# Kernel tuning notes

Measured on AMD Instinct MI355X. Metric: run time of the kernel, lower is better.

The kernel has to match this reference:

```python
import jax, jax.numpy as jnp
import numpy as np
import math

IMAGE_SIZE = 300
STEPS = [16, 32, 64, 100, 150, 300]
MIN_SIZES = [60, 105, 150, 195, 240, 285]
MAX_SIZES = [105, 150, 195, 240, 285, 330]
ASPECT_RATIOS = [2, 3]
SCORE_THRESH = 0.02
NMS_THRESH = 0.45
POST_NMS_TOP_N = 100
VAR_XY, VAR_WH = 0.1, 0.2
BATCH, NUM_CLASSES = 16, 201


def _make_priors():
    # SSD-style anchor generation in (cx, cy, w, h), relative coords.
    priors = []
    for k, step in enumerate(STEPS):
        f = math.ceil(IMAGE_SIZE / step)
        s = MIN_SIZES[k] / IMAGE_SIZE
        sp = math.sqrt(MIN_SIZES[k] * MAX_SIZES[k]) / IMAGE_SIZE
        for i in range(f):
            for j in range(f):
                cx = (j + 0.5) * step / IMAGE_SIZE
                cy = (i + 0.5) * step / IMAGE_SIZE
                priors.append([cx, cy, s, s])
                priors.append([cx, cy, sp, sp])
                for ar in ASPECT_RATIOS:
                    r = math.sqrt(ar)
                    priors.append([cx, cy, s * r, s / r])
                    priors.append([cx, cy, s / r, s * r])
    return np.asarray(priors, dtype=np.float32)  # [3000, 4]


def setup_inputs() -> dict:
    key = jax.random.key(0)
    k1, k2 = jax.random.split(key)
    priors = jnp.asarray(_make_priors())  # [P, 4]
    P = priors.shape[0]
    pred_bbox_deltas = jax.random.normal(k1, (BATCH, P, 4), dtype=jnp.float32)
    objectness = jax.random.normal(k2, (BATCH, P, NUM_CLASSES), dtype=jnp.float32)
    return {"pred_bbox_deltas": pred_bbox_deltas, "objectness": objectness, "priors": priors}


def reference(pred_bbox_deltas, objectness, priors):
    # Eval path of MultiBoxHeads.filter_priors: softmax -> box decode ->
    # score filter -> class-aware (batched) NMS -> top-N, padded to fixed size.
    P = priors.shape[0]
    C = objectness.shape[-1]
    probs = jax.nn.softmax(objectness, axis=-1)  # [B, P, C]

    # BoxCoder.decode with variances (0.1, 0.2); priors are (cx, cy, w, h).
    pxy, pwh = priors[:, :2], priors[:, 2:]
    xy = pred_bbox_deltas[..., :2] * VAR_XY * pwh + pxy  # [B, P, 2]
    wh = jnp.exp(pred_bbox_deltas[..., 2:] * VAR_WH) * pwh
    decoded = jnp.concatenate([xy - 0.5 * wh, xy + 0.5 * wh], axis=-1)  # [B, P, 4] xyxy

    # Per-candidate class labels (background class 0 dropped), shared across images.
    labels = jnp.broadcast_to(jnp.arange(1, C), (P, C - 1)).reshape(-1)  # [P*(C-1)] int

    def nms_image(dec, prob):
        scores = prob[:, 1:].reshape(-1)  # [P*(C-1)]
        boxes = jnp.broadcast_to(dec[:, None, :], (P, C - 1, 4)).reshape(-1, 4)
        s = jnp.where(scores > SCORE_THRESH, scores, -1.0)
        # batched_nms trick: offset boxes by label so classes never overlap.
        off = jnp.max(boxes) + 1.0
        bo = boxes + labels.astype(boxes.dtype)[:, None] * off
        areas = (bo[:, 2] - bo[:, 0]) * (bo[:, 3] - bo[:, 1])

        def step(s, _):
            i = jnp.argmax(s)
            sc = s[i]
            b = bo[i]
            ix1 = jnp.maximum(bo[:, 0], b[0])
            iy1 = jnp.maximum(bo[:, 1], b[1])
            ix2 = jnp.minimum(bo[:, 2], b[2])
            iy2 = jnp.minimum(bo[:, 3], b[3])
            inter = jnp.clip(ix2 - ix1, 0.0) * jnp.clip(iy2 - iy1, 0.0)
            iou = inter / (areas + areas[i] - inter)
            s = jnp.where(iou > NMS_THRESH, -1.0, s).at[i].set(-1.0)
            return s, (i, sc)

        _, (idx, sc) = jax.lax.scan(step, s, None, length=POST_NMS_TOP_N)
        ok = sc > SCORE_THRESH  # slots that hold real detections
        b_out = jnp.where(ok[:, None], jnp.clip(boxes[idx], 0.0, 1.0), 0.0)  # parse() clamp
        s_out = jnp.where(ok, sc, 0.0)
        l_out = jnp.where(ok, labels[idx].astype(boxes.dtype), 0.0)
        # [K, 6] = (x1, y1, x2, y2, score, label); zero rows are padding.
        return jnp.concatenate([b_out, s_out[:, None], l_out[:, None]], axis=-1)

    return jax.vmap(nms_image)(decoded, probs)  # [B, POST_NMS_TOP_N, 6]
```

## Files before the change

kernel.cpp:

```cpp
#include <hip/hip_runtime.h>
#include <cfloat>
#include <cstdint>

#define BATCH 16
#define PRIORS 3000
#define NCLS 201
#define NLBL 200
#define TOPN 100
#define SCORE_THR 0.02f
#define NMS_THR 0.45f

#define FPPB 16
#define FBLK ((PRIORS + FPPB - 1) / FPPB)
#define SEGW 64
#define SEGS (FBLK * 4)
#define SLOTS (SEGS * SEGW)
#define HOTW 8
#define OVF_CAP 1024
#define T0 0.08f

#define NMS_T 1024
#define NBINS 1024
#define HCAP 512
#define SB_BASE 0x3CA3

__device__ __forceinline__ int key_stratum(uint64_t k) {
    int s = (int)(k >> 48) - SB_BASE;
    return s < 0 ? 0 : (s > NBINS - 1 ? NBINS - 1 : s);
}

__device__ __forceinline__ void softmax4(
    const float* __restrict__ obj, int b, int pbase, int lane,
    bool pv[4], float e0[4], float e1[4], float e2[4], float e3[4],
    float inv[4])
{
    float v0[4], v1[4], v2[4], v3[4];
#pragma unroll
    for (int pp = 0; pp < 4; ++pp) {
        int p = pbase + pp;
        pv[pp] = (p < PRIORS);
        const float* x = obj + ((size_t)b * PRIORS + (pv[pp] ? p : PRIORS - 1)) * NCLS;
        v0[pp] = x[lane];
        v1[pp] = x[lane + 64];
        v2[pp] = x[lane + 128];
        v3[pp] = (lane + 192 < NCLS) ? x[lane + 192] : -FLT_MAX;
    }
    float mx[4];
#pragma unroll
    for (int pp = 0; pp < 4; ++pp)
        mx[pp] = fmaxf(fmaxf(v0[pp], v1[pp]), fmaxf(v2[pp], v3[pp]));
    for (int d = 32; d > 0; d >>= 1) {
#pragma unroll
        for (int pp = 0; pp < 4; ++pp)
            mx[pp] = fmaxf(mx[pp], __shfl_xor(mx[pp], d, 64));
    }
    float se[4];
#pragma unroll
    for (int pp = 0; pp < 4; ++pp) {
        e0[pp] = expf(v0[pp] - mx[pp]);
        e1[pp] = expf(v1[pp] - mx[pp]);
        e2[pp] = expf(v2[pp] - mx[pp]);
        e3[pp] = (lane + 192 < NCLS) ? expf(v3[pp] - mx[pp]) : 0.0f;
        se[pp] = e0[pp] + e1[pp] + e2[pp] + e3[pp];
    }
    for (int d = 32; d > 0; d >>= 1) {
#pragma unroll
        for (int pp = 0; pp < 4; ++pp)
            se[pp] += __shfl_xor(se[pp], d, 64);
    }
#pragma unroll
    for (int pp = 0; pp < 4; ++pp) inv[pp] = 1.0f / se[pp];
}

__global__ __launch_bounds__(256) void score_filter_kernel(
    const float* __restrict__ obj,
    uint64_t*    __restrict__ hotS,
    int*         __restrict__ flags)
{
    const int b    = blockIdx.y;
    const int wave = threadIdx.x >> 6;
    const int lane = threadIdx.x & 63;
    const int segId = blockIdx.x * 4 + wave;
    uint64_t* myhot = hotS + ((size_t)b * SEGS + segId) * HOTW;
    const int pbase = blockIdx.x * FPPB + wave * 4;

    bool pv[4]; float e0[4], e1[4], e2[4], e3[4], inv[4];
    softmax4(obj, b, pbase, lane, pv, e0, e1, e2, e3, inv);

    int hcur = 0;
#pragma unroll
    for (int pp = 0; pp < 4; ++pp) {
        float ev[4] = { e0[pp], e1[pp], e2[pp], e3[pp] };
#pragma unroll
        for (int k = 0; k < 4; ++k) {
            int c = lane + 64 * k;
            float prob = ev[k] * inv[pp];
            bool hotp = pv[pp] && (c >= 1) && (c < NCLS) && (prob > T0);
            uint64_t hmask = __ballot(hotp);
            if (hotp) {
                uint32_t oid = (uint32_t)((pbase + pp) * NLBL + (c - 1));
                uint64_t key = ((uint64_t)__float_as_uint(prob) << 32)
                             | (uint64_t)(0xFFFFFFFFu - oid);
                int hidx = hcur + (int)__popcll(hmask & ((1ull << lane) - 1ull));
                if (hidx < HOTW) myhot[hidx] = key;
                else flags[b] = 1;
            }
            hcur += (int)__popcll(hmask);
        }
    }
    if (lane < HOTW && lane >= (hcur < HOTW ? hcur : HOTW)) myhot[lane] = 0ull;
}

__device__ __forceinline__ void sort512_desc(const uint64_t* skey,
                                             uint64_t K[8], int lane)
{
#pragma unroll
    for (int r = 0; r < 8; ++r) K[r] = skey[r * 64 + lane];
#pragma unroll
    for (int k2 = 2; k2 <= 512; k2 <<= 1) {
#pragma unroll
        for (int j2 = k2 >> 1; j2 >= 64; j2 >>= 1) {
            int j2r = j2 >> 6;
#pragma unroll
            for (int r = 0; r < 8; ++r) {
                if ((r & j2r) == 0) {
                    int rp = r | j2r;
                    bool up = ((((r << 6) + lane) & k2) == 0);
                    uint64_t a = K[r], bb = K[rp];
                    uint64_t mxk = a > bb ? a : bb;
                    uint64_t mnk = a > bb ? bb : a;
                    K[r]  = up ? mxk : mnk;
                    K[rp] = up ? mnk : mxk;
                }
            }
        }
#pragma unroll
        for (int j2 = ((k2 >> 1) < 32 ? (k2 >> 1) : 32); j2 >= 1; j2 >>= 1) {
#pragma unroll
            for (int r = 0; r < 8; ++r) {
                uint64_t o = __shfl_xor((unsigned long long)K[r], j2, 64);
                bool up = ((((r << 6) + lane) & k2) == 0);
                bool lower = ((lane & j2) == 0);
                K[r] = (up == lower) ? (K[r] > o ? K[r] : o)
                                     : (K[r] < o ? K[r] : o);
            }
        }
    }
}

__device__ __forceinline__ int scan_sorted_w0(
    const uint64_t K[8], int b, const float4* __restrict__ dbox, float ofb,
    float4* abox, float* aarea, int na, float* __restrict__ out, int lane)
{
#pragma unroll
    for (int r = 0; r < 8; ++r) {
        if (na >= TOPN) break;
        uint64_t myk = K[r];
        bool valid = (myk != 0ull);
        uint32_t oid = 0xFFFFFFFFu - (uint32_t)myk;
        int p = valid ? (int)(oid / NLBL) : 0;
        int c = valid ? ((int)(oid - (uint32_t)p * NLBL) + 1) : 1;
        float4 db = dbox[p];
        float lof = (float)c * ofb;
        float qx1 = db.x + lof, qy1 = db.y + lof;
        float qx2 = db.z + lof, qy2 = db.w + lof;
        float aq = (qx2 - qx1) * (qy2 - qy1);
        bool dead = false;
        for (int l = 0; l < na; ++l) {
            float4 a = abox[l];
            float ix1 = fmaxf(qx1, a.x), iy1 = fmaxf(qy1, a.y);
            float ix2 = fminf(qx2, a.z), iy2 = fminf(qy2, a.w);
            float inter = fmaxf(ix2 - ix1, 0.0f) * fmaxf(iy2 - iy1, 0.0f);
            float iou = inter / (aq + aarea[l] - inter);
            if (iou > NMS_THR) dead = true;
        }
        uint64_t alive = __ballot(valid && !dead);
        while (alive != 0ull && na < TOPN) {
            int j = __ffsll((unsigned long long)alive) - 1;
            float ax1 = __shfl(qx1, j, 64);
            float ay1 = __shfl(qy1, j, 64);
            float ax2 = __shfl(qx2, j, 64);
            float ay2 = __shfl(qy2, j, 64);
            float aa  = __shfl(aq,  j, 64);
            if (lane == j) {
                abox[na]  = make_float4(qx1, qy1, qx2, qy2);
                aarea[na] = aq;
                float* o = out + ((size_t)b * TOPN + na) * 6;
                o[0] = fminf(fmaxf(db.x, 0.0f), 1.0f);
                o[1] = fminf(fmaxf(db.y, 0.0f), 1.0f);
                o[2] = fminf(fmaxf(db.z, 0.0f), 1.0f);
                o[3] = fminf(fmaxf(db.w, 0.0f), 1.0f);
                o[4] = __uint_as_float((uint32_t)(myk >> 32));
                o[5] = (float)c;
            }
            na++;
            bool mine = ((alive >> lane) & 1ull) != 0ull;
            bool drop = (lane == j);
            if (mine && !drop) {
                float ix1 = fmaxf(qx1, ax1), iy1 = fmaxf(qy1, ay1);
                float ix2 = fminf(qx2, ax2), iy2 = fminf(qy2, ay2);
                float inter = fmaxf(ix2 - ix1, 0.0f) * fmaxf(iy2 - iy1, 0.0f);
                float iou = inter / (aq + aa - inter);
                if (iou > NMS_THR) drop = true;
            }
            alive = __ballot(mine && !drop);
        }
    }
    return na;
}

__device__ __forceinline__ int scan_step_w0(
    uint64_t key, int b, const float4* __restrict__ dbox, float ofb,
    float4* abox, float* aarea, int na, float* __restrict__ out, int lane)
{
    uint32_t oid = 0xFFFFFFFFu - (uint32_t)key;
    int p = (int)(oid / NLBL);
    int c = (int)(oid - (uint32_t)p * NLBL) + 1;
    float4 db = dbox[p];
    float lo = (float)c * ofb;
    float qx1 = db.x + lo, qy1 = db.y + lo;
    float qx2 = db.z + lo, qy2 = db.w + lo;
    float aq = (qx2 - qx1) * (qy2 - qy1);
    bool sup = false;
    for (int l = lane; l < na; l += 64) {
        float4 a = abox[l];
        float ix1 = fmaxf(qx1, a.x), iy1 = fmaxf(qy1, a.y);
        float ix2 = fminf(qx2, a.z), iy2 = fminf(qy2, a.w);
        float inter = fmaxf(ix2 - ix1, 0.0f) * fmaxf(iy2 - iy1, 0.0f);
        float iou = inter / (aq + aarea[l] - inter);
        if (iou > NMS_THR) sup = true;
    }
    if (__ballot(sup) == 0ull) {
        if (lane == 0) {
            abox[na]  = make_float4(qx1, qy1, qx2, qy2);
            aarea[na] = aq;
            float* o = out + ((size_t)b * TOPN + na) * 6;
            o[0] = fminf(fmaxf(db.x, 0.0f), 1.0f);
            o[1] = fminf(fmaxf(db.y, 0.0f), 1.0f);
            o[2] = fminf(fmaxf(db.z, 0.0f), 1.0f);
            o[3] = fminf(fmaxf(db.w, 0.0f), 1.0f);
            o[4] = __uint_as_float((uint32_t)(key >> 32));
            o[5] = (float)c;
        }
        __threadfence_block();
        return na + 1;
    }
    return na;
}

__global__ __launch_bounds__(NMS_T) void nms_kernel(
    const float*    __restrict__ deltas,
    const float*    __restrict__ priors,
    const float*    __restrict__ obj,
    const uint64_t* __restrict__ hotS,
    const int*      __restrict__ flags,
    uint64_t*       __restrict__ segWS,
    uint64_t*       __restrict__ ovfWS,
    float*          __restrict__ out)
{
    __shared__ float4   dbox[PRIORS];
    __shared__ int      sufx[NBINS];
    __shared__ uint64_t skey[HCAP];
    __shared__ float4   qbox[HCAP];
    __shared__ float    qarea[HCAP];
    __shared__ uint64_t adjB[8 * HCAP];
    __shared__ float4   abox[112];
    __shared__ float    aarea[112];
    __shared__ uint64_t rk[NMS_T / 64];
    __shared__ float    wredF[NMS_T / 64];
    __shared__ int      wtotS[NMS_T / 64];
    __shared__ int      carryS[NMS_T / 64];
    __shared__ int cntC, ovfC, loS, naS;
    __shared__ uint64_t fkS;

    const int b    = blockIdx.x;
    const int tid  = threadIdx.x;
    const int wave = tid >> 6;
    const int lane = tid & 63;
    const uint64_t* hslots = hotS + (size_t)b * SEGS * HOTW;
    uint64_t* slots = segWS + (size_t)b * SLOTS;
    uint64_t* ovfp  = ovfWS + (size_t)b * OVF_CAP;

    if (tid == 0) { cntC = 0; naS = 0; }
    if (lane == 0) wredF[wave] = -FLT_MAX;
    __syncthreads();

    for (int j = tid; j < SEGS * HOTW; j += NMS_T) {
        uint64_t k = (j < SEGS * HOTW) ? hslots[j] : 0ull;
        uint64_t m = __ballot(k != 0ull);
        if (m) {
            int base = 0;
            if (lane == 0) base = atomicAdd(&cntC, (int)__popcll(m));
            base = __shfl(base, 0, 64);
            if (k) {
                int i = base + (int)__popcll(m & ((1ull << lane) - 1ull));
                if (i < HCAP) skey[i] = k;
            }
        }
    }
    __syncthreads();
    int hc = cntC;
    bool fast = (flags[b] == 0) && (hc <= HCAP);
    bool decoded = false;

    if (fast) {
        if (tid < HCAP && tid >= hc) skey[tid] = 0ull;
        __syncthreads();
        if (wave == 0) {
            uint64_t K[8];
            sort512_desc(skey, K, lane);
#pragma unroll
            for (int r = 0; r < 8; ++r) skey[r * 64 + lane] = K[r];
        } else {
            int base0 = (wave - 1) * 200;
            float lmax = -FLT_MAX;
            for (int p = base0 + lane; p < base0 + 200; p += 64) {
                float4 d4 = ((const float4*)deltas)[(size_t)b * PRIORS + p];
                float4 pr = ((const float4*)priors)[p];
                float cx = d4.x * 0.1f * pr.z + pr.x;
                float cy = d4.y * 0.1f * pr.w + pr.y;
                float w  = expf(d4.z * 0.2f) * pr.z;
                float h  = expf(d4.w * 0.2f) * pr.w;
                float x1 = cx - 0.5f * w, y1 = cy - 0.5f * h;
                float x2 = cx + 0.5f * w, y2 = cy + 0.5f * h;
                dbox[p] = make_float4(x1, y1, x2, y2);
                lmax = fmaxf(lmax, fmaxf(fmaxf(x1, y1), fmaxf(x2, y2)));
            }
            for (int d = 32; d > 0; d >>= 1)
                lmax = fmaxf(lmax, __shfl_xor(lmax, d, 64));
            if (lane == 0) wredF[wave] = lmax;
        }
        decoded = true;
        __syncthreads();

        float v = wredF[lane & 15];
        for (int d = 8; d > 0; d >>= 1) v = fmaxf(v, __shfl_xor(v, d, 64));
        float ofb = v + 1.0f;

        if (tid < HCAP) {
            uint64_t k = skey[tid];
            bool valid = (k != 0ull);
            uint32_t oid = 0xFFFFFFFFu - (uint32_t)k;
            int p = valid ? (int)(oid / NLBL) : 0;
            int c = valid ? ((int)(oid - (uint32_t)p * NLBL) + 1) : 1;
            float4 db = dbox[p];
            float lof = (float)c * ofb;
            float4 q = make_float4(db.x + lof, db.y + lof,
                                   db.z + lof, db.w + lof);
            qbox[tid]  = q;
            qarea[tid] = (q.z - q.x) * (q.w - q.y);
        }
        for (int i = tid; i < 8 * HCAP; i += NMS_T) adjB[i] = 0ull;
        __syncthreads();

        int hcw = (hc + 63) >> 6;
        int P2  = (hcw * (hcw + 1)) >> 1;
        for (int pair = wave; pair < P2; pair += NMS_T / 64) {
            int wj = 0;
            while ((((wj + 1) * (wj + 2)) >> 1) <= pair) ++wj;
            int wi = pair - ((wj * (wj + 1)) >> 1);
            int j  = (wj << 6) + lane;
            float4 qj = qbox[j];
            float  aj = qarea[j];
            int ib = wi << 6;
            uint64_t m = 0ull;
#pragma unroll 8
            for (int i = 0; i < 64; ++i) {
                float4 qi = qbox[ib + i];
                float ix1 = fmaxf(qj.x, qi.x), iy1 = fmaxf(qj.y, qi.y);
                float ix2 = fminf(qj.z, qi.z), iy2 = fminf(qj.w, qi.w);
                float inter = fmaxf(ix2 - ix1, 0.0f) * fmaxf(iy2 - iy1, 0.0f);
                float iou = inter / (aj + qarea[ib + i] - inter);
                m |= (uint64_t)(iou > NMS_THR) << i;
            }
            if (wi == wj)
                m &= (lane == 63) ? ~0ull : ((1ull << (lane + 1)) - 1ull);
            adjB[wi * HCAP + j] = m;
        }
        if (wave == 0 && lane < 8) rk[lane] = 0ull;
        __syncthreads();

        if (wave == 0) {
            uint64_t accwA[8];
#pragma unroll
            for (int w = 0; w < 8; ++w) accwA[w] = 0ull;
            int na = 0;
#pragma unroll
            for (int w = 0; w < 8; ++w) {
                if (w < hcw && na < TOPN) {
                    int nInW = hc - (w << 6);
                    uint64_t init = (nInW >= 64) ? ~0ull
                                  : (nInW > 0 ? ((1ull << nInW) - 1ull) : 0ull);
                    uint64_t deadOr = 0ull;
#pragma unroll
                    for (int wp = 0; wp < w; ++wp)
                        deadOr |= adjB[wp * HCAP + (w << 6) + lane] & accwA[wp];
                    uint64_t mycol = adjB[w * HCAP + (w << 6) + lane];
                    uint64_t rem = init & ~__ballot(deadOr != 0ull);
                    uint64_t acc = 0ull;
                    while (rem != 0ull && na < TOPN) {
                        int rr = __ffsll((unsigned long long)rem) - 1;
                        acc |= 1ull << rr;
                        ++na;
                        rem &= ~__ballot(((mycol >> rr) & 1ull) != 0ull);
                    }
                    accwA[w] = acc;
                    if (lane == 0) rk[w] = acc;
                }
            }
            if (lane == 0) naS = na;
        }
        __syncthreads();

        if (tid < HCAP) {
            int w = tid >> 6, rr = tid & 63;
            uint64_t aw = rk[w];
            if ((aw >> rr) & 1ull) {
                int idx = (int)__popcll(aw & ((1ull << rr) - 1ull));
                for (int k = 0; k < w; ++k) idx += (int)__popcll(rk[k]);
                uint64_t myk = skey[tid];
                uint32_t oid = 0xFFFFFFFFu - (uint32_t)myk;
                int p = (int)(oid / NLBL);
                int c = (int)(oid - (uint32_t)p * NLBL) + 1;
                float4 db = dbox[p];
                float* o = out + ((size_t)b * TOPN + idx) * 6;
                o[0] = fminf(fmaxf(db.x, 0.0f), 1.0f);
                o[1] = fminf(fmaxf(db.y, 0.0f), 1.0f);
                o[2] = fminf(fmaxf(db.z, 0.0f), 1.0f);
                o[3] = fminf(fmaxf(db.w, 0.0f), 1.0f);
                o[4] = __uint_as_float((uint32_t)(myk >> 32));
                o[5] = (float)c;
            }
        }
        __syncthreads();
    }

    if (naS < TOPN) {
        if (tid == 0) ovfC = 0;
        __syncthreads();
        for (int u = wave; u < SEGS; u += NMS_T / 64) {
            int fb = u >> 2, vw = u & 3;
            int pbase = fb * FPPB + vw * 4;
            uint64_t* myseg = slots + (size_t)u * SEGW;
            bool pv[4]; float e0[4], e1[4], e2[4], e3[4], inv[4];
            softmax4(obj, b, pbase, lane, pv, e0, e1, e2, e3, inv);
            int cursor = 0;
#pragma unroll
            for (int pp = 0; pp < 4; ++pp) {
                float ev[4] = { e0[pp], e1[pp], e2[pp], e3[pp] };
#pragma unroll
                for (int k = 0; k < 4; ++k) {
                    int c = lane + 64 * k;
                    float prob = ev[k] * inv[pp];
                    bool pass = pv[pp] && (c >= 1) && (c < NCLS) && (prob > SCORE_THR);
                    uint64_t mask = __ballot(pass);
                    if (pass) {
                        uint32_t oid = (uint32_t)((pbase + pp) * NLBL + (c - 1));
                        uint64_t key = ((uint64_t)__float_as_uint(prob) << 32)
                                     | (uint64_t)(0xFFFFFFFFu - oid);
                        int idx = cursor + (int)__popcll(mask & ((1ull << lane) - 1ull));
                        if (idx < SEGW) {
                            myseg[idx] = key;
                        } else {
                            int gi = atomicAdd(&ovfC, 1);
                            if (gi < OVF_CAP) ovfp[gi] = key;
                        }
                    }
                    cursor += (int)__popcll(mask);
                }
            }
            if (lane >= (cursor < SEGW ? cursor : SEGW)) myseg[lane] = 0ull;
        }
        __threadfence_block();
        __syncthreads();
        int n_ovf = ovfC; if (n_ovf > OVF_CAP) n_ovf = OVF_CAP;

        if (!decoded) {
            float lmax = -FLT_MAX;
            for (int p = tid; p < PRIORS; p += NMS_T) {
                float4 d4 = ((const float4*)deltas)[(size_t)b * PRIORS + p];
                float4 pr = ((const float4*)priors)[p];
                float cx = d4.x * 0.1f * pr.z + pr.x;
                float cy = d4.y * 0.1f * pr.w + pr.y;
                float w  = expf(d4.z * 0.2f) * pr.z;
                float h  = expf(d4.w * 0.2f) * pr.w;
                float x1 = cx - 0.5f * w, y1 = cy - 0.5f * h;
                float x2 = cx + 0.5f * w, y2 = cy + 0.5f * h;
                dbox[p] = make_float4(x1, y1, x2, y2);
                lmax = fmaxf(lmax, fmaxf(fmaxf(x1, y1), fmaxf(x2, y2)));
            }
            for (int d = 32; d > 0; d >>= 1)
                lmax = fmaxf(lmax, __shfl_xor(lmax, d, 64));
            if (lane == 0) wredF[wave] = lmax;
        }
        sufx[tid] = 0;
        if (tid == 0) naS = 0;
        __syncthreads();
        for (int j = tid; j < SLOTS; j += NMS_T) {
            uint64_t k = slots[j];
            if (k) atomicAdd(&sufx[key_stratum(k)], 1);
        }
        for (int j = tid; j < n_ovf; j += NMS_T) {
            uint64_t k = ovfp[j];
            if (k) atomicAdd(&sufx[key_stratum(k)], 1);
        }
        __syncthreads();
        {
            int v = sufx[64 * wave + lane];
            int s = v;
            for (int d = 1; d < 64; d <<= 1) {
                int t = __shfl_down(s, d, 64);
                if (lane + d < 64) s += t;
            }
            if (lane == 0) wtotS[wave] = s;
            __syncthreads();
            if (wave == 0 && lane < NMS_T / 64) {
                int tv = wtotS[lane];
                int ts = tv;
                for (int d = 1; d < NMS_T / 64; d <<= 1) {
                    int t = __shfl_down(ts, d, 64);
                    if (lane + d < NMS_T / 64) ts += t;
                }
                carryS[lane] = ts - tv;
            }
            __syncthreads();
            sufx[64 * wave + lane] = s + carryS[wave];
        }
        int curHi = NBINS;
        for (;;) {
            __syncthreads();
            int naCur = naS;
            int A = (curHi < NBINS) ? sufx[curHi] : 0;
            int remaining = sufx[0] - A;
            if (naCur >= TOPN || remaining <= 0 || curHi <= 0) break;
            int target = A + HCAP;
            if (tid == 0) { loS = curHi; cntC = 0; }
            __syncthreads();
            if (tid < curHi) {
                if (sufx[tid] <= target && (tid == 0 || sufx[tid - 1] > target))
                    loS = tid;
            }
            __syncthreads();
            int lo = loS;

            if (lo < curHi) {
                for (int j = tid; j < SLOTS; j += NMS_T) {
                    uint64_t k = slots[j];
                    if (k) {
                        int s = key_stratum(k);
                        if (s >= lo && s < curHi) {
                            int i = atomicAdd(&cntC, 1);
                            if (i < HCAP) skey[i] = k;
                        }
                    }
                }
                for (int j = tid; j < n_ovf; j += NMS_T) {
                    uint64_t k = ovfp[j];
                    if (k) {
                        int s = key_stratum(k);
                        if (s >= lo && s < curHi) {
                            int i = atomicAdd(&cntC, 1);
                            if (i < HCAP) skey[i] = k;
                        }
                    }
                }
                __syncthreads();
                if (tid < HCAP && tid >= cntC) skey[tid] = 0ull;
                __syncthreads();
                if (wave == 0) {
                    uint64_t K[8];
                    sort512_desc(skey, K, lane);
                    float ofb;
                    {
                        float v = (lane < NMS_T / 64) ? wredF[lane] : -FLT_MAX;
                        for (int d = 32; d > 0; d >>= 1) v = fmaxf(v, __shfl_xor(v, d, 64));
                        ofb = v + 1.0f;
                    }
                    int na = scan_sorted_w0(K, b, dbox, ofb, abox, aarea, naS, out, lane);
                    if (lane == 0) naS = na;
                }
                curHi = lo;
            } else {
                float ofbT;
                {
                    float v = (lane < NMS_T / 64) ? wredF[lane] : -FLT_MAX;
                    for (int d = 32; d > 0; d >>= 1) v = fmaxf(v, __shfl_xor(v, d, 64));
                    ofbT = v + 1.0f;
                }
                int s = curHi - 1;
                uint64_t lastK = ~0ull;
                for (;;) {
                    __syncthreads();
                    if (naS >= TOPN) break;
                    uint64_t bk = 0ull;
                    for (int j = tid; j < SLOTS; j += NMS_T) {
                        uint64_t k = slots[j];
                        if (k && key_stratum(k) == s && k < lastK && k > bk) bk = k;
                    }
                    for (int j = tid; j < n_ovf; j += NMS_T) {
                        uint64_t k = ovfp[j];
                        if (k && key_stratum(k) == s && k < lastK && k > bk) bk = k;
                    }
                    for (int d = 32; d > 0; d >>= 1) {
                        uint64_t o = __shfl_xor((unsigned long long)bk, d, 64);
                        bk = (o > bk) ? o : bk;
                    }
                    if (lane == 0) rk[wave] = bk;
                    __syncthreads();
                    if (tid == 0) {
                        uint64_t fk = rk[0];
                        for (int w = 1; w < NMS_T / 64; ++w) fk = (rk[w] > fk) ? rk[w] : fk;
                        fkS = fk;
                    }
                    __syncthreads();
                    uint64_t fk = fkS;
                    if (fk == 0ull) break;
                    if (wave == 0) {
                        int nal = naS;
                        nal = scan_step_w0(fk, b, dbox, ofbT, abox, aarea, nal, out, lane);
                        if (lane == 0) naS = nal;
                    }
                    lastK = fk;
                }
                curHi = s;
            }
        }
    }
    __syncthreads();
    int naF = naS;
    for (int idx = tid; idx < (TOPN - naF) * 6; idx += NMS_T)
        out[(size_t)b * TOPN * 6 + (size_t)naF * 6 + idx] = 0.0f;
}

extern "C" void kernel_launch(void* const* d_in, const int* in_sizes, int n_in,
                              void* d_out, int out_size, void* d_ws, size_t ws_size,
                              hipStream_t stream)
{
    const float* deltas = (const float*)d_in[0];
    const float* obj    = (const float*)d_in[1];
    const float* priors = (const float*)d_in[2];
    float* out = (float*)d_out;

    char* ws = (char*)d_ws;
    int*      flags = (int*)ws;
    uint64_t* hotA  = (uint64_t*)(ws + 256);
    uint64_t* segA  = hotA + (size_t)BATCH * SEGS * HOTW;
    uint64_t* ovfA  = segA + (size_t)BATCH * SLOTS;

    hipMemsetAsync(ws, 0, 64, stream);
    dim3 fg(FBLK, BATCH, 1);
    score_filter_kernel<<<fg, 256, 0, stream>>>(obj, hotA, flags);
    nms_kernel<<<BATCH, NMS_T, 0, stream>>>(deltas, priors, obj, hotA, flags,
                                            segA, ovfA, out);
}
```

Before: 125.5 us.

## Fuse score filter and NMS into one kernel with last-block election

Merges the softmax/score-filter kernel and the per-image NMS kernel into a single launch. Each block filters 64 priors with 1024 threads, then an atomic counter per image elects the last finishing block to run NMS, removing a kernel launch boundary. To fit shared memory, the decoded box array is dropped on the fast path (boxes are recomputed from global deltas/priors when needed) and a union buffer is shared between the slow-path decoded boxes and the adjacency/query arrays. The NMS tail now runs in whichever block finishes last, and the fast path pays extra global loads and exp per box lookup.

```diff
diff --git a/kernel.cpp b/kernel.cpp
--- a/kernel.cpp
+++ b/kernel.cpp
@@ -10,10 +10,11 @@
 #define SCORE_THR 0.02f
 #define NMS_THR 0.45f
 
-#define FPPB 16
-#define FBLK ((PRIORS + FPPB - 1) / FPPB)
+#define PPB 64
+#define FBLK2 ((PRIORS + PPB - 1) / PPB)
+#define WPB 16
 #define SEGW 64
-#define SEGS (FBLK * 4)
+#define SEGS (FBLK2 * WPB)
 #define SLOTS (SEGS * SEGW)
 #define HOTW 8
 #define OVF_CAP 1024
@@ -27,6 +28,20 @@
 __device__ __forceinline__ int key_stratum(uint64_t k) {
     int s = (int)(k >> 48) - SB_BASE;
     return s < 0 ? 0 : (s > NBINS - 1 ? NBINS - 1 : s);
+}
+
+__device__ __forceinline__ float4 decode_box(
+    const float* __restrict__ deltas, const float* __restrict__ priors,
+    int b, int p)
+{
+    float4 d4 = ((const float4*)deltas)[(size_t)b * PRIORS + p];
+    float4 pr = ((const float4*)priors)[p];
+    float cx = d4.x * 0.1f * pr.z + pr.x;
+    float cy = d4.y * 0.1f * pr.w + pr.y;
+    float w  = expf(d4.z * 0.2f) * pr.z;
+    float h  = expf(d4.w * 0.2f) * pr.w;
+    return make_float4(cx - 0.5f * w, cy - 0.5f * h,
+                       cx + 0.5f * w, cy + 0.5f * h);
 }
 
 __device__ __forceinline__ void softmax4(
@@ -70,45 +85,6 @@
     }
 #pragma unroll
     for (int pp = 0; pp < 4; ++pp) inv[pp] = 1.0f / se[pp];
-}
-
-__global__ __launch_bounds__(256) void score_filter_kernel(
-    const float* __restrict__ obj,
-    uint64_t*    __restrict__ hotS,
-    int*         __restrict__ flags)
-{
-    const int b    = blockIdx.y;
-    const int wave = threadIdx.x >> 6;
-    const int lane = threadIdx.x & 63;
-    const int segId = blockIdx.x * 4 + wave;
-    uint64_t* myhot = hotS + ((size_t)b * SEGS + segId) * HOTW;
-    const int pbase = blockIdx.x * FPPB + wave * 4;
-
-    bool pv[4]; float e0[4], e1[4], e2[4], e3[4], inv[4];
-    softmax4(obj, b, pbase, lane, pv, e0, e1, e2, e3, inv);
-
-    int hcur = 0;
-#pragma unroll
-    for (int pp = 0; pp < 4; ++pp) {
-        float ev[4] = { e0[pp], e1[pp], e2[pp], e3[pp] };
-#pragma unroll
-        for (int k = 0; k < 4; ++k) {
-            int c = lane + 64 * k;
-            float prob = ev[k] * inv[pp];
-            bool hotp = pv[pp] && (c >= 1) && (c < NCLS) && (prob > T0);
-            uint64_t hmask = __ballot(hotp);
-            if (hotp) {
-                uint32_t oid = (uint32_t)((pbase + pp) * NLBL + (c - 1));
-                uint64_t key = ((uint64_t)__float_as_uint(prob) << 32)
-                             | (uint64_t)(0xFFFFFFFFu - oid);
-                int hidx = hcur + (int)__popcll(hmask & ((1ull << lane) - 1ull));
-                if (hidx < HOTW) myhot[hidx] = key;
-                else flags[b] = 1;
-            }
-            hcur += (int)__popcll(hmask);
-        }
-    }
-    if (lane < HOTW && lane >= (hcur < HOTW ? hcur : HOTW)) myhot[lane] = 0ull;
 }
 
 __device__ __forceinline__ void sort512_desc(const uint64_t* skey,
@@ -149,7 +125,7 @@
 }
 
 __device__ __forceinline__ int scan_sorted_w0(
-    const uint64_t K[8], int b, const float4* __restrict__ dbox, float ofb,
+    const uint64_t K[8], int b, const float4* dbox, float ofb,
     float4* abox, float* aarea, int na, float* __restrict__ out, int lane)
 {
 #pragma unroll
@@ -210,7 +186,7 @@
 }
 
 __device__ __forceinline__ int scan_step_w0(
-    uint64_t key, int b, const float4* __restrict__ dbox, float ofb,
+    uint64_t key, int b, const float4* dbox, float ofb,
     float4* abox, float* aarea, int na, float* __restrict__ out, int lane)
 {
     uint32_t oid = 0xFFFFFFFFu - (uint32_t)key;
@@ -248,35 +224,78 @@
     return na;
 }
 
-__global__ __launch_bounds__(NMS_T) void nms_kernel(
+__global__ __launch_bounds__(NMS_T) void fused_kernel(
     const float*    __restrict__ deltas,
     const float*    __restrict__ priors,
     const float*    __restrict__ obj,
-    const uint64_t* __restrict__ hotS,
-    const int*      __restrict__ flags,
+    uint64_t*       __restrict__ hotS,
+    int*            __restrict__ flags,
+    int*            __restrict__ done,
     uint64_t*       __restrict__ segWS,
     uint64_t*       __restrict__ ovfWS,
     float*          __restrict__ out)
 {
-    __shared__ float4   dbox[PRIORS];
+    __shared__ __align__(16) char uMem[48 * 1024];
+    uint64_t* adjB  = (uint64_t*)uMem;
+    float4*   qbox  = (float4*)(uMem + 32 * 1024);
+    float*    qarea = (float*)(uMem + 40 * 1024);
+    float4*   dboxF = (float4*)uMem;
+    __shared__ uint64_t skey[HCAP];
     __shared__ int      sufx[NBINS];
-    __shared__ uint64_t skey[HCAP];
-    __shared__ float4   qbox[HCAP];
-    __shared__ float    qarea[HCAP];
-    __shared__ uint64_t adjB[8 * HCAP];
     __shared__ float4   abox[112];
     __shared__ float    aarea[112];
     __shared__ uint64_t rk[NMS_T / 64];
     __shared__ float    wredF[NMS_T / 64];
     __shared__ int      wtotS[NMS_T / 64];
     __shared__ int      carryS[NMS_T / 64];
-    __shared__ int cntC, ovfC, loS, naS;
+    __shared__ int cntC, ovfC, loS, naS, electedS;
     __shared__ uint64_t fkS;
 
-    const int b    = blockIdx.x;
+    const int b    = blockIdx.y;
     const int tid  = threadIdx.x;
     const int wave = tid >> 6;
     const int lane = tid & 63;
+
+    {
+        const int segId = blockIdx.x * WPB + wave;
+        const int pbase = blockIdx.x * PPB + wave * 4;
+        uint64_t* myhot = hotS + ((size_t)b * SEGS + segId) * HOTW;
+
+        bool pv[4]; float e0[4], e1[4], e2[4], e3[4], inv[4];
+        softmax4(obj, b, pbase, lane, pv, e0, e1, e2, e3, inv);
+
+        int hcur = 0;
+#pragma unroll
+        for (int pp = 0; pp < 4; ++pp) {
+            float ev[4] = { e0[pp], e1[pp], e2[pp], e3[pp] };
+#pragma unroll
+            for (int k = 0; k < 4; ++k) {
+                int c = lane + 64 * k;
+                float prob = ev[k] * inv[pp];
+                bool hotp = pv[pp] && (c >= 1) && (c < NCLS) && (prob > T0);
+                uint64_t hmask = __ballot(hotp);
+                if (hotp) {
+                    uint32_t oid = (uint32_t)((pbase + pp) * NLBL + (c - 1));
+                    uint64_t key = ((uint64_t)__float_as_uint(prob) << 32)
+                                 | (uint64_t)(0xFFFFFFFFu - oid);
+                    int hidx = hcur + (int)__popcll(hmask & ((1ull << lane) - 1ull));
+                    if (hidx < HOTW) myhot[hidx] = key;
+                    else flags[b] = 1;
+                }
+                hcur += (int)__popcll(hmask);
+            }
+        }
+        if (lane < HOTW && lane >= (hcur < HOTW ? hcur : HOTW)) myhot[lane] = 0ull;
+    }
+
+    __threadfence();
+    __syncthreads();
+    if (tid == 0)
+        electedS = (atomicAdd(&done[b], 1) == FBLK2 - 1) ? 1 : 0;
+    __syncthreads();
+    if (!electedS) return;
+    __threadfence();
+
     const uint64_t* hslots = hotS + (size_t)b * SEGS * HOTW;
     uint64_t* slots = segWS + (size_t)b * SLOTS;
     uint64_t* ovfp  = ovfWS + (size_t)b * OVF_CAP;
@@ -286,7 +305,7 @@
     __syncthreads();
 
     for (int j = tid; j < SEGS * HOTW; j += NMS_T) {
-        uint64_t k = (j < SEGS * HOTW) ? hslots[j] : 0ull;
+        uint64_t k = hslots[j];
         uint64_t m = __ballot(k != 0ull);
         if (m) {
             int base = 0;
@@ -301,7 +320,6 @@
     __syncthreads();
     int hc = cntC;
     bool fast = (flags[b] == 0) && (hc <= HCAP);
-    bool decoded = false;
 
     if (fast) {
         if (tid < HCAP && tid >= hc) skey[tid] = 0ull;
@@ -315,22 +333,13 @@
             int base0 = (wave - 1) * 200;
             float lmax = -FLT_MAX;
             for (int p = base0 + lane; p < base0 + 200; p += 64) {
-                float4 d4 = ((const float4*)deltas)[(size_t)b * PRIORS + p];
-                float4 pr = ((const float4*)priors)[p];
-                float cx = d4.x * 0.1f * pr.z + pr.x;
-                float cy = d4.y * 0.1f * pr.w + pr.y;
-                float w  = expf(d4.z * 0.2f) * pr.z;
-                float h  = expf(d4.w * 0.2f) * pr.w;
-                float x1 = cx - 0.5f * w, y1 = cy - 0.5f * h;
-                float x2 = cx + 0.5f * w, y2 = cy + 0.5f * h;
-                dbox[p] = make_float4(x1, y1, x2, y2);
-                lmax = fmaxf(lmax, fmaxf(fmaxf(x1, y1), fmaxf(x2, y2)));
+                float4 d = decode_box(deltas, priors, b, p);
+                lmax = fmaxf(lmax, fmaxf(fmaxf(d.x, d.y), fmaxf(d.z, d.w)));
             }
             for (int d = 32; d > 0; d >>= 1)
                 lmax = fmaxf(lmax, __shfl_xor(lmax, d, 64));
             if (lane == 0) wredF[wave] = lmax;
         }
-        decoded = true;
         __syncthreads();
 
         float v = wredF[lane & 15];
@@ -343,7 +352,7 @@
             uint32_t oid = 0xFFFFFFFFu - (uint32_t)k;
             int p = valid ? (int)(oid / NLBL) : 0;
             int c = valid ? ((int)(oid - (uint32_t)p * NLBL) + 1) : 1;
-            float4 db = dbox[p];
+            float4 db = decode_box(deltas, priors, b, p);
             float lof = (float)c * ofb;
             float4 q = make_float4(db.x + lof, db.y + lof,
                                    db.z + lof, db.w + lof);
@@ -422,7 +431,7 @@
                 uint32_t oid = 0xFFFFFFFFu - (uint32_t)myk;
                 int p = (int)(oid / NLBL);
                 int c = (int)(oid - (uint32_t)p * NLBL) + 1;
-                float4 db = dbox[p];
+                float4 db = decode_box(deltas, priors, b, p);
                 float* o = out + ((size_t)b * TOPN + idx) * 6;
                 o[0] = fminf(fmaxf(db.x, 0.0f), 1.0f);
                 o[1] = fminf(fmaxf(db.y, 0.0f), 1.0f);
@@ -439,8 +448,8 @@
         if (tid == 0) ovfC = 0;
         __syncthreads();
         for (int u = wave; u < SEGS; u += NMS_T / 64) {
-            int fb = u >> 2, vw = u & 3;
-            int pbase = fb * FPPB + vw * 4;
+            int fb = u >> 4, vw = u & 15;
+            int pbase = fb * PPB + vw * 4;
             uint64_t* myseg = slots + (size_t)u * SEGW;
             bool pv[4]; float e0[4], e1[4], e2[4], e3[4], inv[4];
             softmax4(obj, b, pbase, lane, pv, e0, e1, e2, e3, inv);
@@ -475,19 +484,12 @@
         __syncthreads();
         int n_ovf = ovfC; if (n_ovf > OVF_CAP) n_ovf = OVF_CAP;
 
-        if (!decoded) {
+        {
             float lmax = -FLT_MAX;
             for (int p = tid; p < PRIORS; p += NMS_T) {
-                float4 d4 = ((const float4*)deltas)[(size_t)b * PRIORS + p];
-                float4 pr = ((const float4*)priors)[p];
-                float cx = d4.x * 0.1f * pr.z + pr.x;
-                float cy = d4.y * 0.1f * pr.w + pr.y;
-                float w  = expf(d4.z * 0.2f) * pr.z;
-                float h  = expf(d4.w * 0.2f) * pr.w;
-                float x1 = cx - 0.5f * w, y1 = cy - 0.5f * h;
-                float x2 = cx + 0.5f * w, y2 = cy + 0.5f * h;
-                dbox[p] = make_float4(x1, y1, x2, y2);
-                lmax = fmaxf(lmax, fmaxf(fmaxf(x1, y1), fmaxf(x2, y2)));
+                float4 d = decode_box(deltas, priors, b, p);
+                dboxF[p] = d;
+                lmax = fmaxf(lmax, fmaxf(fmaxf(d.x, d.y), fmaxf(d.z, d.w)));
             }
             for (int d = 32; d > 0; d >>= 1)
                 lmax = fmaxf(lmax, __shfl_xor(lmax, d, 64));
@@ -576,7 +578,7 @@
                         for (int d = 32; d > 0; d >>= 1) v = fmaxf(v, __shfl_xor(v, d, 64));
                         ofb = v + 1.0f;
                     }
-                    int na = scan_sorted_w0(K, b, dbox, ofb, abox, aarea, naS, out, lane);
+                    int na = scan_sorted_w0(K, b, dboxF, ofb, abox, aarea, naS, out, lane);
                     if (lane == 0) naS = na;
                 }
                 curHi = lo;
@@ -617,7 +619,7 @@
                     if (fk == 0ull) break;
                     if (wave == 0) {
                         int nal = naS;
-                        nal = scan_step_w0(fk, b, dbox, ofbT, abox, aarea, nal, out, lane);
+                        nal = scan_step_w0(fk, b, dboxF, ofbT, abox, aarea, nal, out, lane);
                         if (lane == 0) naS = nal;
                     }
                     lastK = fk;
@@ -643,13 +645,13 @@
 
     char* ws = (char*)d_ws;
     int*      flags = (int*)ws;
+    int*      done  = (int*)(ws + 64);
     uint64_t* hotA  = (uint64_t*)(ws + 256);
     uint64_t* segA  = hotA + (size_t)BATCH * SEGS * HOTW;
     uint64_t* ovfA  = segA + (size_t)BATCH * SLOTS;
 
-    hipMemsetAsync(ws, 0, 64, stream);
-    dim3 fg(FBLK, BATCH, 1);
-    score_filter_kernel<<<fg, 256, 0, stream>>>(obj, hotA, flags);
-    nms_kernel<<<BATCH, NMS_T, 0, stream>>>(deltas, priors, obj, hotA, flags,
-                                            segA, ovfA, out);
-}
+    hipMemsetAsync(ws, 0, 128, stream);
+    dim3 fg(FBLK2, BATCH, 1);
+    fused_kernel<<<fg, NMS_T, 0, stream>>>(deltas, priors, obj, hotA,
+                                           flags, done, segA, ovfA, out);
+}
```

Measured after the change: 336.0 us. +167.8%, slower.
